# Performance work log

Hardware: AMD Instinct MI355X
Metric: run time of the kernel (lower is better)

Reference implementation:

```python
import jax, jax.numpy as jnp
import numpy as np

B, C, H, W = 64, 1, 256, 256        # x shape; seq_len = C*H = 256, input_dim = W = 256
E, HID, L, NCLS = 512, 1024, 2, 10


def _lstm_layer(xs, h0, c0, Wx, bx, Wh, bh):
    """xs: [S,B,in] -> ys: [S,B,HID]. Gate order: f, i, g(candidate), o."""
    def step(carry, xt):
        h, c = carry
        gates = xt @ Wx + bx + h @ Wh + bh            # [B, 4*HID] (fuses 8 tiny Linears into 2 GEMMs)
        f, i, g, o = jnp.split(gates, 4, axis=-1)
        f = jax.nn.sigmoid(f)
        i = jax.nn.sigmoid(i)
        g = jnp.tanh(g)
        o = jax.nn.sigmoid(o)
        c = f * c + i * g
        h = o * jnp.tanh(c)
        return (h, c), h
    (hT, cT), ys = jax.lax.scan(step, (h0, c0), xs)
    return ys


def setup_inputs() -> dict:
    key = jax.random.key(0)
    ks = jax.random.split(key, 16)
    s = 0.02
    inp = {
        "x": jax.random.normal(ks[0], (B, C, H, W), jnp.float32),
        "h0": jax.random.normal(ks[1], (L, B, HID), jnp.float32),
        "c0": jax.random.normal(ks[2], (L, B, HID), jnp.float32),
        "W_enc": jax.random.normal(ks[3], (W, E), jnp.float32) * s,
        "b_enc": jnp.zeros((E,), jnp.float32),
        "alpha": jnp.float32(0.25),  # PReLU default single-parameter weight
        "Wx0": jax.random.normal(ks[4], (E, 4 * HID), jnp.float32) * s,
        "bx0": jnp.zeros((4 * HID,), jnp.float32),
        "Wh0": jax.random.normal(ks[5], (HID, 4 * HID), jnp.float32) * s,
        "bh0": jnp.zeros((4 * HID,), jnp.float32),
        "Wx1": jax.random.normal(ks[6], (HID, 4 * HID), jnp.float32) * s,
        "bx1": jnp.zeros((4 * HID,), jnp.float32),
        "Wh1": jax.random.normal(ks[7], (HID, 4 * HID), jnp.float32) * s,
        "bh1": jnp.zeros((4 * HID,), jnp.float32),
        "W_cls": jax.random.normal(ks[8], (HID, NCLS), jnp.float32) * s,
        "b_cls": jnp.zeros((NCLS,), jnp.float32),
    }
    return inp


def reference(x, h0, c0, W_enc, b_enc, alpha, Wx0, bx0, Wh0, bh0,
              Wx1, bx1, Wh1, bh1, W_cls, b_cls):
    b, c, h, w = x.shape
    x = x.reshape(b, c * h, w)                    # [B, S, input_dim]
    e = x @ W_enc + b_enc                         # encoder Linear
    e = jnp.where(e >= 0, e, alpha * e)           # PReLU (single shared alpha)
    xs = jnp.swapaxes(e, 0, 1)                    # [S, B, E] for scan
    ys = _lstm_layer(xs, h0[0], c0[0], Wx0, bx0, Wh0, bh0)
    ys = _lstm_layer(ys, h0[1], c0[1], Wx1, bx1, Wh1, bh1)
    return ys[-1] @ W_cls + b_cls                 # classify last timestep -> [B, 10]
```

## Files before the change

### kernel.cpp

```cpp
#include <hip/hip_runtime.h>
#include <hip/hip_bf16.h>
#include <cstddef>


using short8 = __attribute__((ext_vector_type(8))) short;
using f32x4  = __attribute__((ext_vector_type(4))) float;

#define LD8(p) (*reinterpret_cast<const short8*>(p))

__device__ __forceinline__ float sigmoidf_(float x) {
    return 1.f / (1.f + __expf(-x));
}
__device__ __forceinline__ unsigned short f2bf(float x) {
    union { float f; unsigned u; } v; v.f = x;
    unsigned r = v.u + 0x7fffu + ((v.u >> 16) & 1u);
    return (unsigned short)(r >> 16);
}
__device__ __forceinline__ float bf2f(unsigned short h) {
    union { unsigned u; float f; } v; v.u = ((unsigned)h) << 16;
    return v.f;
}

__global__ __launch_bounds__(256) void enc_gemm_k(
    const float* __restrict__ A, const float* __restrict__ B,
    unsigned short* __restrict__ Ef,
    const float* __restrict__ bias1, const float* __restrict__ alphap,
    int M, int N, int K, int sB, int sS)
{
    __shared__ float As[128][17];
    __shared__ float Bs[16][64];
    const int tid = threadIdx.x;
    const int tx = tid & 15, ty = tid >> 4;
    const int rb = blockIdx.y * 128;
    const int cb = blockIdx.x * 64;

    float acc[8][4];
#pragma unroll
    for (int i = 0; i < 8; ++i)
#pragma unroll
        for (int j = 0; j < 4; ++j) acc[i][j] = 0.f;

    const int nk = K >> 4;
    for (int kt = 0; kt < nk; ++kt) {
        const int k0 = kt << 4;
        __syncthreads();
        {
            const int row = tid >> 2, k4 = tid & 3;
#pragma unroll
            for (int h = 0; h < 2; ++h) {
                const int r = rb + row + h * 64;
                const float4 v = *reinterpret_cast<const float4*>(
                    &A[(size_t)(r & 63) * sB + (size_t)(r >> 6) * sS + k0 + k4 * 4]);
                As[row + h * 64][k4 * 4 + 0] = v.x;
                As[row + h * 64][k4 * 4 + 1] = v.y;
                As[row + h * 64][k4 * 4 + 2] = v.z;
                As[row + h * 64][k4 * 4 + 3] = v.w;
            }
        }
        {
            const int bk = tid >> 4, c4 = tid & 15;
            *reinterpret_cast<float4*>(&Bs[bk][c4 * 4]) =
                *reinterpret_cast<const float4*>(
                    &B[(size_t)(k0 + bk) * N + cb + c4 * 4]);
        }
        __syncthreads();
#pragma unroll
        for (int k = 0; k < 16; ++k) {
            float a[8];
#pragma unroll
            for (int i = 0; i < 8; ++i) a[i] = As[ty * 8 + i][k];
            const float4 bv = *reinterpret_cast<const float4*>(&Bs[k][tx * 4]);
#pragma unroll
            for (int i = 0; i < 8; ++i) {
                acc[i][0] = fmaf(a[i], bv.x, acc[i][0]);
                acc[i][1] = fmaf(a[i], bv.y, acc[i][1]);
                acc[i][2] = fmaf(a[i], bv.z, acc[i][2]);
                acc[i][3] = fmaf(a[i], bv.w, acc[i][3]);
            }
        }
    }

    float bsum[4];
#pragma unroll
    for (int j = 0; j < 4; ++j) bsum[j] = bias1[cb + tx * 4 + j];
    const float alpha = alphap[0];
    const int k0c = cb + tx * 4;
    const int s = k0c >> 5, kg = (k0c >> 3) & 3, e0 = k0c & 7;
#pragma unroll
    for (int i = 0; i < 8; ++i) {
        const int r = rb + ty * 8 + i;
        const int t = r >> 6, b = r & 63;
        const int ln = (b & 15) + 16 * kg, nj = b >> 4;
        unsigned short hs[4], ls[4];
#pragma unroll
        for (int j = 0; j < 4; ++j) {
            float v = acc[i][j] + bsum[j];
            v = (v >= 0.f) ? v : alpha * v;
            hs[j] = f2bf(v);
            ls[j] = f2bf(v - bf2f(hs[j]));
        }
        uint2 hp, lp;
        hp.x = (unsigned)hs[0] | ((unsigned)hs[1] << 16);
        hp.y = (unsigned)hs[2] | ((unsigned)hs[3] << 16);
        lp.x = (unsigned)ls[0] | ((unsigned)ls[1] << 16);
        lp.y = (unsigned)ls[2] | ((unsigned)ls[3] << 16);
        const size_t base =
            ((((size_t)t * 32 + s) * 4 + nj) * 64 + ln) * 8 + e0;
        *reinterpret_cast<uint2*>(Ef + base) = hp;
        *reinterpret_cast<uint2*>(Ef + base + 32768) = lp;
    }
}

__global__ __launch_bounds__(256) void wprep_k(
    const float* __restrict__ Wa, const float* __restrict__ Wb,
    unsigned short* __restrict__ Wf, int NS)
{
    __shared__ float tl[32][65];
    const int k0 = blockIdx.x * 32, j0 = blockIdx.y * 64;
    const int tid = threadIdx.x;
    {
        const int kk = tid >> 3, jq = tid & 7;
        const int k = k0 + kk;
        const float* src = (k < 1024) ? &Wa[(size_t)k * 4096]
                                      : &Wb[(size_t)(k - 1024) * 4096];
#pragma unroll
        for (int h = 0; h < 2; ++h) {
            const float4 v = *reinterpret_cast<const float4*>(
                &src[j0 + jq * 8 + h * 4]);
            tl[kk][jq * 8 + h * 4 + 0] = v.x; tl[kk][jq * 8 + h * 4 + 1] = v.y;
            tl[kk][jq * 8 + h * 4 + 2] = v.z; tl[kk][jq * 8 + h * 4 + 3] = v.w;
        }
    }
    __syncthreads();
    const int j = tid >> 2, kg = tid & 3;
    const int jg = j0 + j;
    const int g = jg >> 10, cc = jg & 1023;
    const int lb = cc >> 3, c = cc & 7;
    const int rloc = g * 8 + c;
    const int mi = rloc >> 4, r16 = rloc & 15;
    const int lane = r16 + 16 * kg;
    const int s = k0 >> 5;
    short8 hv, lv;
#pragma unroll
    for (int e = 0; e < 8; ++e) {
        const float x = tl[kg * 8 + e][j];
        const unsigned short h = f2bf(x);
        hv[e] = (short)h;
        lv[e] = (short)f2bf(x - bf2f(h));
    }
    const size_t oH = ((((size_t)lb * 2 + 0) * NS + s) * 2 + mi) * 512 + (size_t)lane * 8;
    const size_t oL = ((((size_t)lb * 2 + 1) * NS + s) * 2 + mi) * 512 + (size_t)lane * 8;
    *reinterpret_cast<short8*>(Wf + oH) = hv;
    *reinterpret_cast<short8*>(Wf + oL) = lv;
}

__global__ __launch_bounds__(256) void hsplit_k(
    const float* __restrict__ hrow, unsigned short* __restrict__ dst)
{
    const int idx = blockIdx.x * 256 + threadIdx.x;
    const int b = idx >> 7, gc = idx & 127;
    const int k = gc * 8;
    short8 hv, lv;
#pragma unroll
    for (int e = 0; e < 8; ++e) {
        const float x = hrow[(size_t)b * 1024 + k + e];
        const unsigned short h = f2bf(x);
        hv[e] = (short)h;
        lv[e] = (short)f2bf(x - bf2f(h));
    }
    const int s = k >> 5, kg = (k >> 3) & 3, nj = b >> 4;
    const int l = (b & 15) + 16 * kg;
    const size_t oH = (((size_t)(0 * 32 + s) * 4 + nj) * 64 + l) * 8;
    const size_t oL = (((size_t)(1 * 32 + s) * 4 + nj) * 64 + l) * 8;
    *reinterpret_cast<short8*>(dst + oH) = hv;
    *reinterpret_cast<short8*>(dst + oL) = lv;
}

__global__ __launch_bounds__(256) void bsum_k(
    const float* __restrict__ bx, const float* __restrict__ bh,
    float* __restrict__ out)
{
    const int r = blockIdx.x * 256 + threadIdx.x;
    const int lb = r >> 5, rl = r & 31;
    const int g = rl >> 3, c = rl & 7;
    const int j = g * 1024 + lb * 8 + c;
    out[r] = bx[j] + bh[j];
}

__device__ __forceinline__ void poll_flags(unsigned* bar, int base,
                                           unsigned need, int tid) {
    if (tid < 128) {
        unsigned* p = bar + (size_t)(base + tid) * 32;
        while (__hip_atomic_load(p, __ATOMIC_RELAXED,
                                 __HIP_MEMORY_SCOPE_AGENT) < need)
            __builtin_amdgcn_s_sleep(1);
    }
    __syncthreads();
}

__global__ __launch_bounds__(512, 2) void fused_lstm_k(
    const unsigned short* __restrict__ Ef,
    const unsigned short* __restrict__ Wf0,
    const unsigned short* __restrict__ Wf1,
    unsigned short* __restrict__ Y0, unsigned short* __restrict__ H1,
    const float* __restrict__ c0, const float* __restrict__ bsum0p,
    const float* __restrict__ bsum1p, float* __restrict__ hst1,
    unsigned* bar)
{
    __shared__ float Pred[8][32][66];
    __shared__ unsigned short hasmH[64][8];
    __shared__ unsigned short hasmL[64][8];

    const int tid = threadIdx.x;
    const int lane = tid & 63;
    const int w = tid >> 6;
    const int bid = blockIdx.x;
    const int layer = bid >> 7;
    const int lb = bid & 127;

    const int NS = layer ? 64 : 48;
    const int nEx = layer ? 4 : 2;
    const int wNS = NS * 1024;

    const unsigned short* Wf = layer ? Wf1 : Wf0;
    const unsigned short* wB =
        Wf + (size_t)lb * 2 * NS * 1024 + (size_t)lane * 8;

    short8 w00r[8], w01r[8], w10r[8], w11r[8];
#pragma unroll
    for (int i = 0; i < 8; ++i)
        if (i < 4 + nEx) {
            const int sg = (i < 4)
                ? (w * 4 + i)
                : (layer ? (32 + w * 4 + (i - 4)) : (32 + w * 2 + (i - 4)));
            const unsigned short* wp = wB + (size_t)sg * 1024;
            w00r[i] = LD8(wp);        w01r[i] = LD8(wp + 512);
            w10r[i] = LD8(wp + wNS);  w11r[i] = LD8(wp + wNS + 512);
        }

    const int col = w;
    float c_ = c0[(size_t)layer * 65536 + (size_t)lane * 1024 + lb * 8 + col];
    const float* bsB = layer ? bsum1p : bsum0p;
    float bs[4];
#pragma unroll
    for (int g = 0; g < 4; ++g) bs[g] = bsB[lb * 32 + g * 8 + col];

#define MM(mi, nj, HH, HL)                                                     \
    acc[mi][nj] = __builtin_amdgcn_mfma_f32_16x16x32_bf16(                     \
        (mi) ? w01r[i] : w00r[i], HH, acc[mi][nj], 0, 0, 0);                   \
    acc[mi][nj] = __builtin_amdgcn_mfma_f32_16x16x32_bf16(                     \
        (mi) ? w01r[i] : w00r[i], HL, acc[mi][nj], 0, 0, 0);                   \
    acc[mi][nj] = __builtin_amdgcn_mfma_f32_16x16x32_bf16(                     \
        (mi) ? w11r[i] : w10r[i], HH, acc[mi][nj], 0, 0, 0);
#define SUBTILE(hp, po)                                                        \
    {                                                                          \
        const short8 h0v = LD8(hp),        h1v = LD8(hp + 512);                \
        const short8 h2v = LD8(hp + 1024), h3v = LD8(hp + 1536);               \
        const short8 l0v = LD8(hp + po),        l1v = LD8(hp + po + 512);      \
        const short8 l2v = LD8(hp + po + 1024), l3v = LD8(hp + po + 1536);     \
        MM(0, 0, h0v, l0v)  MM(0, 1, h1v, l1v)                                 \
        MM(0, 2, h2v, l2v)  MM(0, 3, h3v, l3v)                                 \
        MM(1, 0, h0v, l0v)  MM(1, 1, h1v, l1v)                                 \
        MM(1, 2, h2v, l2v)  MM(1, 3, h3v, l3v)                                 \
    }

    for (int r = 1; r <= 257; ++r) {
        const bool act = layer ? (r >= 2) : (r <= 256);
        if (act) {
            const int t = layer ? r - 2 : r - 1;
            const unsigned short* hOwn =
                (layer ? H1 : Y0) + (size_t)t * 131072 + (size_t)lane * 8;
            const unsigned short* hCross = layer
                ? Y0 + (size_t)(t + 1) * 131072 + (size_t)lane * 8
                : Ef + (size_t)t * 65536 + (size_t)lane * 8;
            const int poCross = layer ? 65536 : 32768;

            f32x4 acc[2][4] = {};

            if (layer) poll_flags(bar, 0, (unsigned)(r - 1), tid);
#pragma unroll
            for (int i = 4; i < 8; ++i)
                if (i < 4 + nEx) {
                    const int cs = layer ? (w * 4 + (i - 4)) : (w * 2 + (i - 4));
                    const unsigned short* hp = hCross + (size_t)cs * 2048;
                    SUBTILE(hp, poCross)
                }

            if (r >= 2) poll_flags(bar, layer ? 128 : 0, (unsigned)(r - 1), tid);
#pragma unroll
            for (int i = 0; i < 4; ++i) {
                const unsigned short* hp = hOwn + (size_t)(w * 4 + i) * 2048;
                SUBTILE(hp, 65536)
            }

            {
                const int rq = (lane >> 4) * 4, cq = lane & 15;
#pragma unroll
                for (int mi = 0; mi < 2; ++mi)
#pragma unroll
                    for (int nj = 0; nj < 4; ++nj)
#pragma unroll
                        for (int rr = 0; rr < 4; ++rr)
                            Pred[w][mi * 16 + rq + rr][nj * 16 + cq] =
                                acc[mi][nj][rr];
            }
            __syncthreads();

            {
                float p[4];
#pragma unroll
                for (int g = 0; g < 4; ++g) {
                    const int row = g * 8 + col;
                    float s0 = 0.f;
#pragma unroll
                    for (int ww = 0; ww < 8; ++ww)
                        s0 += Pred[ww][row][lane];
                    p[g] = s0 + bs[g];
                }
                const float fg = sigmoidf_(p[0]);
                const float ig = sigmoidf_(p[1]);
                const float gg = tanhf(p[2]);
                const float og = sigmoidf_(p[3]);
                c_ = fmaf(fg, c_, ig * gg);
                const float h = og * tanhf(c_);
                const unsigned short hh = f2bf(h);
                hasmH[lane][col] = hh;
                hasmL[lane][col] = f2bf(h - bf2f(hh));
                if (layer && r == 257)
                    hst1[(size_t)(lb * 8 + col) * 64 + lane] = h;
            }
            __syncthreads();

            if (tid < 128) {
                const int p = tid >> 6, b = tid & 63;
                unsigned short* hw =
                    (layer ? H1 : Y0) + (size_t)(t + 1) * 131072;
                const size_t off =
                    (((size_t)(p * 32 + (lb >> 2)) * 4 + (b >> 4)) * 64 +
                     ((b & 15) + 16 * (lb & 3))) * 8;
                const unsigned long long* src =
                    reinterpret_cast<const unsigned long long*>(
                        p ? &hasmL[b][0] : &hasmH[b][0]);
                unsigned long long* dst =
                    reinterpret_cast<unsigned long long*>(hw + off);
                __hip_atomic_store(dst, src[0], __ATOMIC_RELAXED,
                                   __HIP_MEMORY_SCOPE_AGENT);
                __hip_atomic_store(dst + 1, src[1], __ATOMIC_RELAXED,
                                   __HIP_MEMORY_SCOPE_AGENT);
            }
        }

        if (r <= 256) {
            __syncthreads();
            if (tid == 0)
                __hip_atomic_store(bar + (size_t)bid * 32, (unsigned)r,
                                   __ATOMIC_RELAXED, __HIP_MEMORY_SCOPE_AGENT);
        }
    }
#undef SUBTILE
#undef MM
}

__global__ __launch_bounds__(256) void cls_k(
    const float* __restrict__ hfin, const float* __restrict__ Wc,
    const float* __restrict__ bcls, float* __restrict__ out)
{
    __shared__ float red[4][64];
    const int n = blockIdx.x;
    const int lane = threadIdx.x & 63, w = threadIdx.x >> 6;
    float acc = 0.f;
    for (int k = w * 256; k < w * 256 + 256; ++k)
        acc = fmaf(hfin[k * 64 + lane], Wc[k * 10 + n], acc);
    red[w][lane] = acc;
    __syncthreads();
    if (w == 0) {
        out[lane * 10 + n] = red[0][lane] + red[1][lane] + red[2][lane] +
                             red[3][lane] + bcls[n];
    }
}

extern "C" void kernel_launch(void* const* d_in, const int* in_sizes, int n_in,
                              void* d_out, int out_size, void* d_ws,
                              size_t ws_size, hipStream_t stream)
{
    const float* x    = (const float*)d_in[0];
    const float* h0   = (const float*)d_in[1];
    const float* c0   = (const float*)d_in[2];
    const float* Wenc = (const float*)d_in[3];
    const float* benc = (const float*)d_in[4];
    const float* alpha= (const float*)d_in[5];
    const float* Wx0  = (const float*)d_in[6];
    const float* bx0  = (const float*)d_in[7];
    const float* Wh0  = (const float*)d_in[8];
    const float* bh0  = (const float*)d_in[9];
    const float* Wx1  = (const float*)d_in[10];
    const float* bx1  = (const float*)d_in[11];
    const float* Wh1  = (const float*)d_in[12];
    const float* bh1  = (const float*)d_in[13];
    const float* Wcls = (const float*)d_in[14];
    const float* bcls = (const float*)d_in[15];
    float* out = (float*)d_out;

    float* ws = (float*)d_ws;
    size_t off = 0;
    unsigned short* Ef   = (unsigned short*)(ws + off); off += 8388608;
    unsigned short* Wf0  = (unsigned short*)(ws + off); off += 6291456;
    unsigned short* Wf1  = (unsigned short*)(ws + off); off += 8388608;
    unsigned short* Y0   = (unsigned short*)(ws + off); off += 16842752;
    unsigned short* H1   = (unsigned short*)(ws + off); off += 16842752;
    float* bsum0p = ws + off; off += 4096;
    float* bsum1p = ws + off; off += 4096;
    float* hst1   = ws + off; off += 65536;
    unsigned* bars = (unsigned*)(ws + off); off += 8192;

    (void)hipMemsetAsync(bars, 0, 32768, stream);

    enc_gemm_k<<<dim3(8, 128), 256, 0, stream>>>(
        x, Wenc, Ef, benc, alpha, 16384, 512, 256, 65536, 256);
    wprep_k<<<dim3(48, 64), 256, 0, stream>>>(Wh0, Wx0, Wf0, 48);
    wprep_k<<<dim3(64, 64), 256, 0, stream>>>(Wh1, Wx1, Wf1, 64);
    hsplit_k<<<32, 256, 0, stream>>>(h0, Y0);
    hsplit_k<<<32, 256, 0, stream>>>(h0 + 65536, H1);
    bsum_k<<<16, 256, 0, stream>>>(bx0, bh0, bsum0p);
    bsum_k<<<16, 256, 0, stream>>>(bx1, bh1, bsum1p);

    fused_lstm_k<<<256, 512, 0, stream>>>(Ef, Wf0, Wf1, Y0, H1, c0,
                                          bsum0p, bsum1p, hst1, bars);

    cls_k<<<dim3(10), 256, 0, stream>>>(hst1, Wcls, bcls, out);
}
```

Measured before the change: 1.913 ms.

## Move encoder GEMM to split-bf16 MFMA and use per-wave flag polling

Replaces the fp32 SIMT encoder GEMM with a three-term split-bf16 MFMA GEMM, preceded by kernels that split x and the transposed encoder weight into hi/lo bf16 parts. The aim is to cut the encoder matmul's FMA cost, at the price of two extra prep passes and some extra memory traffic. It also swaps the block-wide flag poll plus __syncthreads in the recurrent LSTM kernel for a per-wave poll of only the 16 flags each wave depends on, so waves stop waiting on each other. The split-bf16 scheme drops the lo×lo term, so results may differ slightly from fp32.

```diff
diff --git a/kernel.cpp b/kernel.cpp
--- a/kernel.cpp
+++ b/kernel.cpp
@@ -21,93 +21,169 @@
     return v.f;
 }
 
-__global__ __launch_bounds__(256) void enc_gemm_k(
-    const float* __restrict__ A, const float* __restrict__ B,
-    unsigned short* __restrict__ Ef,
-    const float* __restrict__ bias1, const float* __restrict__ alphap,
-    int M, int N, int K, int sB, int sS)
-{
-    __shared__ float As[128][17];
-    __shared__ float Bs[16][64];
+__global__ __launch_bounds__(256) void xsplit_k(
+    const float* __restrict__ x, unsigned short* __restrict__ Xhi,
+    unsigned short* __restrict__ Xlo)
+{
+    const int idx = blockIdx.x * 256 + threadIdx.x;
+    const int m = idx >> 5, kq = idx & 31;
+    const int b = m & 63, t = m >> 6;
+    const float* src = x + (size_t)b * 65536 + (size_t)t * 256 + kq * 8;
+    short8 hv, lv;
+#pragma unroll
+    for (int e = 0; e < 8; ++e) {
+        const float f = src[e];
+        const unsigned short h = f2bf(f);
+        hv[e] = (short)h;
+        lv[e] = (short)f2bf(f - bf2f(h));
+    }
+    const size_t o = (size_t)m * 256 + kq * 8;
+    *reinterpret_cast<short8*>(Xhi + o) = hv;
+    *reinterpret_cast<short8*>(Xlo + o) = lv;
+}
+
+__global__ __launch_bounds__(256) void bsplitN_k(
+    const float* __restrict__ W, unsigned short* __restrict__ Bhi,
+    unsigned short* __restrict__ Blo, int K, int N)
+{
+    __shared__ float tl[32][65];
+    const int k0 = blockIdx.x * 32, n0 = blockIdx.y * 64;
     const int tid = threadIdx.x;
-    const int tx = tid & 15, ty = tid >> 4;
-    const int rb = blockIdx.y * 128;
-    const int cb = blockIdx.x * 64;
-
-    float acc[8][4];
-#pragma unroll
-    for (int i = 0; i < 8; ++i)
-#pragma unroll
-        for (int j = 0; j < 4; ++j) acc[i][j] = 0.f;
-
-    const int nk = K >> 4;
-    for (int kt = 0; kt < nk; ++kt) {
-        const int k0 = kt << 4;
+    {
+        const int kk = tid >> 3, nq = tid & 7;
+#pragma unroll
+        for (int j = 0; j < 2; ++j) {
+            const float4 v = *reinterpret_cast<const float4*>(
+                &W[(size_t)(k0 + kk) * N + n0 + nq * 8 + j * 4]);
+            tl[kk][nq * 8 + j * 4 + 0] = v.x; tl[kk][nq * 8 + j * 4 + 1] = v.y;
+            tl[kk][nq * 8 + j * 4 + 2] = v.z; tl[kk][nq * 8 + j * 4 + 3] = v.w;
+        }
+    }
+    __syncthreads();
+    const int n = tid >> 2, kq = tid & 3;
+    short8 hv, lv;
+#pragma unroll
+    for (int j = 0; j < 8; ++j) {
+        const float xv = tl[kq * 8 + j][n];
+        const unsigned short h = f2bf(xv);
+        hv[j] = (short)h;
+        lv[j] = (short)f2bf(xv - bf2f(h));
+    }
+    const size_t o = (size_t)(n0 + n) * K + k0 + kq * 8;
+    *reinterpret_cast<short8*>(&Bhi[o]) = hv;
+    *reinterpret_cast<short8*>(&Blo[o]) = lv;
+}
+
+__global__ __launch_bounds__(256) void enc_mfma_k(
+    const unsigned short* __restrict__ Ahi, const unsigned short* __restrict__ Alo,
+    const unsigned short* __restrict__ Bhi, const unsigned short* __restrict__ Blo,
+    unsigned short* __restrict__ Ef, const float* __restrict__ benc,
+    const float* __restrict__ alphap)
+{
+    __shared__ float smemf[10240];
+    unsigned short* const smemh = (unsigned short*)smemf;
+    unsigned short* const As0 = smemh;
+    unsigned short* const As1 = smemh + 5120;
+    unsigned short* const Bs0 = smemh + 10240;
+    unsigned short* const Bs1 = smemh + 15360;
+
+    const int tid = threadIdx.x;
+    const int lane = tid & 63, wid = tid >> 6;
+    const int wm = wid >> 1, wn = wid & 1;
+    const int m0 = blockIdx.y * 128;
+    const int n0 = blockIdx.x * 128;
+    const int K = 256;
+
+    f32x4 acc[4][4] = {};
+
+    const int sr = tid & 127;
+    const int spl = tid >> 7;
+    const unsigned short* Ag = (spl ? Alo : Ahi) + (size_t)(m0 + sr) * K;
+    const unsigned short* Bg = (spl ? Blo : Bhi) + (size_t)(n0 + sr) * K;
+    unsigned short* Asw = (spl ? As1 : As0) + sr * 40;
+    unsigned short* Bsw = (spl ? Bs1 : Bs0) + sr * 40;
+    const int sw = sr & 3;
+
+    const int kg = lane >> 4;
+    const int fr = lane & 15;
+
+    for (int k0 = 0; k0 < K; k0 += 32) {
+        short8 av[4], bv[4];
+#pragma unroll
+        for (int c = 0; c < 4; ++c) {
+            av[c] = LD8(Ag + k0 + c * 8);
+            bv[c] = LD8(Bg + k0 + c * 8);
+        }
         __syncthreads();
-        {
-            const int row = tid >> 2, k4 = tid & 3;
-#pragma unroll
-            for (int h = 0; h < 2; ++h) {
-                const int r = rb + row + h * 64;
-                const float4 v = *reinterpret_cast<const float4*>(
-                    &A[(size_t)(r & 63) * sB + (size_t)(r >> 6) * sS + k0 + k4 * 4]);
-                As[row + h * 64][k4 * 4 + 0] = v.x;
-                As[row + h * 64][k4 * 4 + 1] = v.y;
-                As[row + h * 64][k4 * 4 + 2] = v.z;
-                As[row + h * 64][k4 * 4 + 3] = v.w;
+#pragma unroll
+        for (int c = 0; c < 4; ++c) {
+            *reinterpret_cast<short8*>(Asw + ((c ^ sw) * 8)) = av[c];
+            *reinterpret_cast<short8*>(Bsw + ((c ^ sw) * 8)) = bv[c];
+        }
+        __syncthreads();
+
+        short8 af[2][4], bf[2][4];
+#pragma unroll
+        for (int i = 0; i < 4; ++i) {
+            const int ra = wm * 64 + i * 16 + fr;
+            const int rb = wn * 64 + i * 16 + fr;
+            af[0][i] = LD8(As0 + ra * 40 + ((kg ^ (ra & 3)) * 8));
+            af[1][i] = LD8(As1 + ra * 40 + ((kg ^ (ra & 3)) * 8));
+            bf[0][i] = LD8(Bs0 + rb * 40 + ((kg ^ (rb & 3)) * 8));
+            bf[1][i] = LD8(Bs1 + rb * 40 + ((kg ^ (rb & 3)) * 8));
+        }
+#pragma unroll
+        for (int i = 0; i < 4; ++i)
+#pragma unroll
+            for (int j = 0; j < 4; ++j) {
+                acc[i][j] = __builtin_amdgcn_mfma_f32_16x16x32_bf16(
+                    af[0][i], bf[0][j], acc[i][j], 0, 0, 0);
+                acc[i][j] = __builtin_amdgcn_mfma_f32_16x16x32_bf16(
+                    af[0][i], bf[1][j], acc[i][j], 0, 0, 0);
+                acc[i][j] = __builtin_amdgcn_mfma_f32_16x16x32_bf16(
+                    af[1][i], bf[0][j], acc[i][j], 0, 0, 0);
             }
-        }
-        {
-            const int bk = tid >> 4, c4 = tid & 15;
-            *reinterpret_cast<float4*>(&Bs[bk][c4 * 4]) =
-                *reinterpret_cast<const float4*>(
-                    &B[(size_t)(k0 + bk) * N + cb + c4 * 4]);
-        }
+    }
+    __syncthreads();
+
+    float* slab = smemf + wid * 1040;
+    const int t = (m0 >> 6) + wm;
+    const int fq = lane >> 4;
+    const float alpha = alphap[0];
+#pragma unroll 1
+    for (int j = 0; j < 4; ++j) {
+#pragma unroll
+        for (int i = 0; i < 4; ++i)
+#pragma unroll
+            for (int rr = 0; rr < 4; ++rr)
+                slab[fr * 65 + i * 16 + fq * 4 + rr] = acc[i][j][rr];
         __syncthreads();
-#pragma unroll
-        for (int k = 0; k < 16; ++k) {
-            float a[8];
-#pragma unroll
-            for (int i = 0; i < 8; ++i) a[i] = As[ty * 8 + i][k];
-            const float4 bv = *reinterpret_cast<const float4*>(&Bs[k][tx * 4]);
-#pragma unroll
-            for (int i = 0; i < 8; ++i) {
-                acc[i][0] = fmaf(a[i], bv.x, acc[i][0]);
-                acc[i][1] = fmaf(a[i], bv.y, acc[i][1]);
-                acc[i][2] = fmaf(a[i], bv.z, acc[i][2]);
-                acc[i][3] = fmaf(a[i], bv.w, acc[i][3]);
+        const int b = lane;
+        const int nj = b >> 4;
+#pragma unroll
+        for (int ng = 0; ng < 4; ++ng) {
+            const int n = n0 + wn * 64 + j * 16 + ng * 4;
+            unsigned short hs[4], ls[4];
+#pragma unroll
+            for (int v = 0; v < 4; ++v) {
+                float f = slab[(ng * 4 + v) * 65 + b] + benc[n + v];
+                f = (f >= 0.f) ? f : alpha * f;
+                hs[v] = f2bf(f);
+                ls[v] = f2bf(f - bf2f(hs[v]));
             }
-        }
-    }
-
-    float bsum[4];
-#pragma unroll
-    for (int j = 0; j < 4; ++j) bsum[j] = bias1[cb + tx * 4 + j];
-    const float alpha = alphap[0];
-    const int k0c = cb + tx * 4;
-    const int s = k0c >> 5, kg = (k0c >> 3) & 3, e0 = k0c & 7;
-#pragma unroll
-    for (int i = 0; i < 8; ++i) {
-        const int r = rb + ty * 8 + i;
-        const int t = r >> 6, b = r & 63;
-        const int ln = (b & 15) + 16 * kg, nj = b >> 4;
-        unsigned short hs[4], ls[4];
-#pragma unroll
-        for (int j = 0; j < 4; ++j) {
-            float v = acc[i][j] + bsum[j];
-            v = (v >= 0.f) ? v : alpha * v;
-            hs[j] = f2bf(v);
-            ls[j] = f2bf(v - bf2f(hs[j]));
-        }
-        uint2 hp, lp;
-        hp.x = (unsigned)hs[0] | ((unsigned)hs[1] << 16);
-        hp.y = (unsigned)hs[2] | ((unsigned)hs[3] << 16);
-        lp.x = (unsigned)ls[0] | ((unsigned)ls[1] << 16);
-        lp.y = (unsigned)ls[2] | ((unsigned)ls[3] << 16);
-        const size_t base =
-            ((((size_t)t * 32 + s) * 4 + nj) * 64 + ln) * 8 + e0;
-        *reinterpret_cast<uint2*>(Ef + base) = hp;
-        *reinterpret_cast<uint2*>(Ef + base + 32768) = lp;
+            uint2 hp, lp;
+            hp.x = (unsigned)hs[0] | ((unsigned)hs[1] << 16);
+            hp.y = (unsigned)hs[2] | ((unsigned)hs[3] << 16);
+            lp.x = (unsigned)ls[0] | ((unsigned)ls[1] << 16);
+            lp.y = (unsigned)ls[2] | ((unsigned)ls[3] << 16);
+            const int s = n >> 5, kgn = (n >> 3) & 3, e0 = n & 7;
+            const int ln = (b & 15) + 16 * kgn;
+            const size_t base =
+                ((((size_t)t * 32 + s) * 4 + nj) * 64 + ln) * 8 + e0;
+            *reinterpret_cast<uint2*>(Ef + base) = hp;
+            *reinterpret_cast<uint2*>(Ef + base + 32768) = lp;
+        }
+        __syncthreads();
     }
 }
 
@@ -185,17 +261,6 @@
     const int g = rl >> 3, c = rl & 7;
     const int j = g * 1024 + lb * 8 + c;
     out[r] = bx[j] + bh[j];
-}
-
-__device__ __forceinline__ void poll_flags(unsigned* bar, int base,
-                                           unsigned need, int tid) {
-    if (tid < 128) {
-        unsigned* p = bar + (size_t)(base + tid) * 32;
-        while (__hip_atomic_load(p, __ATOMIC_RELAXED,
-                                 __HIP_MEMORY_SCOPE_AGENT) < need)
-            __builtin_amdgcn_s_sleep(1);
-    }
-    __syncthreads();
 }
 
 __global__ __launch_bounds__(512, 2) void fused_lstm_k(
@@ -263,6 +328,17 @@
         MM(1, 0, h0v, l0v)  MM(1, 1, h1v, l1v)                                 \
         MM(1, 2, h2v, l2v)  MM(1, 3, h3v, l3v)                                 \
     }
+#define WPOLL(baseIdx, need)                                                   \
+    {                                                                          \
+        if (lane < 16) {                                                       \
+            unsigned* p = bar + (size_t)((baseIdx) + lane) * 32;               \
+            while (__hip_atomic_load(p, __ATOMIC_RELAXED,                      \
+                                     __HIP_MEMORY_SCOPE_AGENT) < (need))       \
+                __builtin_amdgcn_s_sleep(1);                                   \
+        }                                                                      \
+        __builtin_amdgcn_wave_barrier();                                       \
+        asm volatile("" ::: "memory");                                         \
+    }
 
     for (int r = 1; r <= 257; ++r) {
         const bool act = layer ? (r >= 2) : (r <= 256);
@@ -277,7 +353,7 @@
 
             f32x4 acc[2][4] = {};
 
-            if (layer) poll_flags(bar, 0, (unsigned)(r - 1), tid);
+            if (layer) WPOLL(w * 16, (unsigned)(r - 1))
 #pragma unroll
             for (int i = 4; i < 8; ++i)
                 if (i < 4 + nEx) {
@@ -286,7 +362,7 @@
                     SUBTILE(hp, poCross)
                 }
 
-            if (r >= 2) poll_flags(bar, layer ? 128 : 0, (unsigned)(r - 1), tid);
+            if (r >= 2) WPOLL((layer ? 128 : 0) + w * 16, (unsigned)(r - 1))
 #pragma unroll
             for (int i = 0; i < 4; ++i) {
                 const unsigned short* hp = hOwn + (size_t)(w * 4 + i) * 2048;
@@ -357,6 +433,7 @@
                                    __ATOMIC_RELAXED, __HIP_MEMORY_SCOPE_AGENT);
         }
     }
+#undef WPOLL
 #undef SUBTILE
 #undef MM
 }
@@ -408,6 +485,10 @@
     unsigned short* Wf1  = (unsigned short*)(ws + off); off += 8388608;
     unsigned short* Y0   = (unsigned short*)(ws + off); off += 16842752;
     unsigned short* H1   = (unsigned short*)(ws + off); off += 16842752;
+    unsigned short* Xhi  = (unsigned short*)(ws + off); off += 2097152;
+    unsigned short* Xlo  = (unsigned short*)(ws + off); off += 2097152;
+    unsigned short* WeThi= (unsigned short*)(ws + off); off += 65536;
+    unsigned short* WeTlo= (unsigned short*)(ws + off); off += 65536;
     float* bsum0p = ws + off; off += 4096;
     float* bsum1p = ws + off; off += 4096;
     float* hst1   = ws + off; off += 65536;
@@ -415,8 +496,10 @@
 
     (void)hipMemsetAsync(bars, 0, 32768, stream);
 
-    enc_gemm_k<<<dim3(8, 128), 256, 0, stream>>>(
-        x, Wenc, Ef, benc, alpha, 16384, 512, 256, 65536, 256);
+    xsplit_k<<<2048, 256, 0, stream>>>(x, Xhi, Xlo);
+    bsplitN_k<<<dim3(8, 8), 256, 0, stream>>>(Wenc, WeThi, WeTlo, 256, 512);
+    enc_mfma_k<<<dim3(4, 128), 256, 0, stream>>>(
+        Xhi, Xlo, WeThi, WeTlo, Ef, benc, alpha);
     wprep_k<<<dim3(48, 64), 256, 0, stream>>>(Wh0, Wx0, Wf0, 48);
     wprep_k<<<dim3(64, 64), 256, 0, stream>>>(Wh1, Wx1, Wf1, 64);
     hsplit_k<<<32, 256, 0, stream>>>(h0, Y0);
```

Result: no change. 1.914 ms, median of 2 (+0.0%).
